# Kernel optimization log

Hardware: AMD Instinct MI355X
Metric: run time of the kernel (lower is better)

## Reference

```python
import jax, jax.numpy as jnp
import numpy as np

B, S, H, N = 1024, 200, 128, 100000  # batch, seq_len, hidden_size, num_item


def setup_inputs() -> dict:
    key = jax.random.key(0)
    ks = jax.random.split(key, 6)
    return {
        "all_memory": jax.random.normal(ks[0], (B, S, H), dtype=jnp.float32),
        "last_memory": jax.random.normal(ks[1], (B, H), dtype=jnp.float32),
        "item_seq": jax.random.randint(ks[2], (B, S), 0, N),
        "mask": jnp.zeros((B, S), dtype=jnp.bool_),
        "Ur_w": jax.random.normal(ks[3], (H, H), dtype=jnp.float32) / np.sqrt(H),
        "Wr_w": jax.random.normal(ks[4], (H, H), dtype=jnp.float32) / np.sqrt(H),
        "Vr_w": jax.random.normal(ks[5], (1, H), dtype=jnp.float32) / np.sqrt(H),
        "Vr_b": jnp.zeros((1,), dtype=jnp.float32),
    }


def reference(all_memory, last_memory, item_seq, mask, Ur_w, Wr_w, Vr_w, Vr_b):
    # torch Linear: y = x @ W.T (+ b). dropout_prob=0 -> identity.
    am = jnp.einsum("bsh,kh->bsk", all_memory, Ur_w)          # [B,S,H]
    lm = jnp.einsum("bh,kh->bk", last_memory, Wr_w)           # [B,H]
    e = jnp.tanh(am + lm[:, None, :])                          # [B,S,H]
    scores = jnp.einsum("bsh,oh->bso", e, Vr_w)[..., 0] + Vr_b  # [B,S]
    scores = jnp.where(mask, jnp.float32(-1e9), scores)
    att = jax.nn.softmax(scores, axis=-1)                      # [B,S]
    # scatter_add along item-id bins per batch row
    rows = jnp.arange(att.shape[0])[:, None]                   # [B,1]
    out = jnp.zeros((att.shape[0], N), dtype=att.dtype)
    out = out.at[rows, item_seq].add(att)                      # [B,N]
    return out
```

## Files before the change

### kernel.cpp

```cpp
#include <hip/hip_runtime.h>
#include <math.h>
#include <stdint.h>

#define BB 1024
#define SS 200
#define HH 128
#define NI 100000

typedef __attribute__((ext_vector_type(8))) short short8;
typedef __attribute__((ext_vector_type(4))) float f32x4;

__device__ __forceinline__ float fast_tanh(float x) {
    float ax = fabsf(x);
    float t = __expf(-2.0f * ax);
    float r = (1.0f - t) / (1.0f + t);
    return copysignf(r, x);
}

__device__ __forceinline__ void split8(const float* __restrict__ p,
                                       short8& hi, short8& lo) {
    const float4* p4 = reinterpret_cast<const float4*>(p);
    float4 x0 = p4[0], x1 = p4[1];
    float v[8] = {x0.x, x0.y, x0.z, x0.w, x1.x, x1.y, x1.z, x1.w};
    #pragma unroll
    for (int j = 0; j < 8; ++j) {
        unsigned u = __float_as_uint(v[j]);
        unsigned short h = (unsigned short)(u >> 16);
        hi[j] = (short)h;
        float r = v[j] - __uint_as_float(((unsigned)h) << 16);
        lo[j] = (short)(__float_as_uint(r) >> 16);
    }
}

__global__ __launch_bounds__(256, 2)
void rrd_mfma_kernel(const float* __restrict__ allm,
                     const float* __restrict__ lastm,
                     const int* __restrict__ item_seq,
                     const unsigned char* __restrict__ mask,
                     const float* __restrict__ Ur,
                     const float* __restrict__ Wr,
                     const float* __restrict__ Vr,
                     const float* __restrict__ Vrb,
                     float* __restrict__ out) {
    const int b = blockIdx.x;
    const int tid = threadIdx.x;
    const int lane = tid & 63;
    const int w = tid >> 6;
    const int col = lane & 15;
    const int quad = lane >> 4;

    __shared__ float s_last[HH];
    __shared__ float s_lm[HH];
    __shared__ float s_vr[HH];
    __shared__ float s_score[256];
    __shared__ float s_red[8];

    if (tid < HH) s_last[tid] = lastm[b * HH + tid];
    else          s_vr[tid - HH] = Vr[tid - HH];
    __syncthreads();

    if (tid < HH) {
        const float4* wrow = reinterpret_cast<const float4*>(Wr + tid * HH);
        const float4* lrow = reinterpret_cast<const float4*>(s_last);
        float4 acc = make_float4(0.f, 0.f, 0.f, 0.f);
        #pragma unroll
        for (int i = 0; i < HH / 4; ++i) {
            float4 wv = wrow[i];
            float4 lv = lrow[i];
            acc.x = fmaf(lv.x, wv.x, acc.x);
            acc.y = fmaf(lv.y, wv.y, acc.y);
            acc.z = fmaf(lv.z, wv.z, acc.z);
            acc.w = fmaf(lv.w, wv.w, acc.w);
        }
        s_lm[tid] = (acc.x + acc.y) + (acc.z + acc.w);
    }
    __syncthreads();

    const int row0 = w * 64;
    #pragma unroll 1
    for (int p = 0; p < 2; ++p) {
        f32x4 C[2][8] = {};
        #pragma unroll 1
        for (int c = 0; c < 4; ++c) {
            short8 Bh[8], Bl[8];
            #pragma unroll
            for (int n = 0; n < 8; ++n) {
                const float* bp = Ur + (size_t)(n * 16 + col) * HH + c * 32 + quad * 8;
                split8(bp, Bh[n], Bl[n]);
            }
            #pragma unroll
            for (int t = 0; t < 2; ++t) {
                int row = row0 + (p * 2 + t) * 16 + col;
                if (row > SS - 1) row = SS - 1;
                const float* ap = allm + ((size_t)b * SS + row) * HH + c * 32 + quad * 8;
                short8 Ah, Al;
                split8(ap, Ah, Al);
                #pragma unroll
                for (int n = 0; n < 8; ++n) {
                    C[t][n] = __builtin_amdgcn_mfma_f32_16x16x32_bf16(Ah, Bh[n], C[t][n], 0, 0, 0);
                    C[t][n] = __builtin_amdgcn_mfma_f32_16x16x32_bf16(Ah, Bl[n], C[t][n], 0, 0, 0);
                    C[t][n] = __builtin_amdgcn_mfma_f32_16x16x32_bf16(Al, Bh[n], C[t][n], 0, 0, 0);
                }
            }
        }
        #pragma unroll
        for (int t = 0; t < 2; ++t) {
            float a0 = 0.f, a1 = 0.f, a2 = 0.f, a3 = 0.f;
            #pragma unroll
            for (int n = 0; n < 8; ++n) {
                float lmc = s_lm[n * 16 + col];
                float vrc = s_vr[n * 16 + col];
                a0 = fmaf(vrc, fast_tanh(C[t][n][0] + lmc), a0);
                a1 = fmaf(vrc, fast_tanh(C[t][n][1] + lmc), a1);
                a2 = fmaf(vrc, fast_tanh(C[t][n][2] + lmc), a2);
                a3 = fmaf(vrc, fast_tanh(C[t][n][3] + lmc), a3);
            }
            #pragma unroll
            for (int off = 1; off < 16; off <<= 1) {
                a0 += __shfl_xor(a0, off, 64);
                a1 += __shfl_xor(a1, off, 64);
                a2 += __shfl_xor(a2, off, 64);
                a3 += __shfl_xor(a3, off, 64);
            }
            if (col == 0) {
                int rb = row0 + (p * 2 + t) * 16 + quad * 4;
                s_score[rb + 0] = a0;
                s_score[rb + 1] = a1;
                s_score[rb + 2] = a2;
                s_score[rb + 3] = a3;
            }
        }
    }

    {
        float4* orow = reinterpret_cast<float4*>(out + (size_t)b * NI);
        const float4 z4 = make_float4(0.f, 0.f, 0.f, 0.f);
        for (int i = tid; i < NI / 4; i += 256) orow[i] = z4;
    }

    __syncthreads();

    const int s = tid;
    float score = s_score[s] + Vrb[0];
    if (s < SS && mask[b * SS + s]) score = -1e9f;

    float v = (s < SS) ? score : -3.0e38f;
    #pragma unroll
    for (int off = 32; off > 0; off >>= 1)
        v = fmaxf(v, __shfl_down(v, off, 64));
    if (lane == 0) s_red[w] = v;
    __syncthreads();
    float m = fmaxf(fmaxf(s_red[0], s_red[1]), fmaxf(s_red[2], s_red[3]));

    float e = (s < SS) ? __expf(score - m) : 0.f;
    float sv = e;
    #pragma unroll
    for (int off = 32; off > 0; off >>= 1)
        sv += __shfl_down(sv, off, 64);
    if (lane == 0) s_red[4 + w] = sv;
    __syncthreads();
    float tot = (s_red[4] + s_red[5]) + (s_red[6] + s_red[7]);

    if (s < SS) {
        float att = e / tot;
        int idx = item_seq[b * SS + s];
        atomicAdd(out + (size_t)b * NI + idx, att);
    }
}

extern "C" void kernel_launch(void* const* d_in, const int* in_sizes, int n_in,
                              void* d_out, int out_size, void* d_ws, size_t ws_size,
                              hipStream_t stream) {
    const float* allm   = (const float*)d_in[0];
    const float* lastm  = (const float*)d_in[1];
    const int*   iseq   = (const int*)d_in[2];
    const unsigned char* mask = (const unsigned char*)d_in[3];
    const float* Ur     = (const float*)d_in[4];
    const float* Wr     = (const float*)d_in[5];
    const float* Vr     = (const float*)d_in[6];
    const float* Vrb    = (const float*)d_in[7];
    float* out          = (float*)d_out;

    rrd_mfma_kernel<<<dim3(BB), dim3(256), 0, stream>>>(
        allm, lastm, iseq, mask, Ur, Wr, Vr, Vrb, out);
}
```

Before: 569.0 us.

## Precompute Wr projection and Ur bf16 hi/lo split in a prep kernel

Adds a prep kernel that computes last_memory@Wr^T for all batches and pre-splits Ur into bf16 hi/lo fragments laid out in MFMA operand order in workspace. The main kernel then loads these ready-made fragments instead of redoing the Wr matvec and the Ur split in each of 1024 blocks. This removes redundant per-block ALU work and Ur reads, at the cost of an extra kernel launch and workspace traffic. It falls back to the old kernel when the workspace is too small.

```diff
diff --git a/kernel.cpp b/kernel.cpp
--- a/kernel.cpp
+++ b/kernel.cpp
@@ -29,6 +29,169 @@
         hi[j] = (short)h;
         float r = v[j] - __uint_as_float(((unsigned)h) << 16);
         lo[j] = (short)(__float_as_uint(r) >> 16);
+    }
+}
+
+__global__ __launch_bounds__(256)
+void rrd_prep_kernel(const float* __restrict__ lastm,
+                     const float* __restrict__ Wr,
+                     const float* __restrict__ Ur,
+                     float* __restrict__ lm_ws,
+                     short* __restrict__ ur_hi,
+                     short* __restrict__ ur_lo) {
+    const int blk = blockIdx.x;
+    const int tid = threadIdx.x;
+    if (blk < 512) {
+        const int gid = blk * 256 + tid;
+        const int b = gid >> 7;
+        const int k = gid & 127;
+        const float4* wrow = reinterpret_cast<const float4*>(Wr + (size_t)k * HH);
+        const float4* lrow = reinterpret_cast<const float4*>(lastm + (size_t)b * HH);
+        float4 acc = make_float4(0.f, 0.f, 0.f, 0.f);
+        #pragma unroll
+        for (int i = 0; i < HH / 4; ++i) {
+            float4 wv = wrow[i];
+            float4 lv = lrow[i];
+            acc.x = fmaf(lv.x, wv.x, acc.x);
+            acc.y = fmaf(lv.y, wv.y, acc.y);
+            acc.z = fmaf(lv.z, wv.z, acc.z);
+            acc.w = fmaf(lv.w, wv.w, acc.w);
+        }
+        lm_ws[gid] = (acc.x + acc.y) + (acc.z + acc.w);
+    } else {
+        const int r = (blk - 512) * 256 + tid;
+        const int c    = r >> 9;
+        const int n    = (r >> 6) & 7;
+        const int quad = (r >> 4) & 3;
+        const int col  = r & 15;
+        const int row = n * 16 + col;
+        const int k0  = c * 32 + quad * 8;
+        short8 hi, lo;
+        split8(Ur + (size_t)row * HH + k0, hi, lo);
+        reinterpret_cast<short8*>(ur_hi)[r] = hi;
+        reinterpret_cast<short8*>(ur_lo)[r] = lo;
+    }
+}
+
+__global__ __launch_bounds__(256, 2)
+void rrd_mfma_kernel_p(const float* __restrict__ allm,
+                       const int* __restrict__ item_seq,
+                       const unsigned char* __restrict__ mask,
+                       const short* __restrict__ ur_hi,
+                       const short* __restrict__ ur_lo,
+                       const float* __restrict__ lm_ws,
+                       const float* __restrict__ Vr,
+                       const float* __restrict__ Vrb,
+                       float* __restrict__ out) {
+    const int b = blockIdx.x;
+    const int tid = threadIdx.x;
+    const int lane = tid & 63;
+    const int w = tid >> 6;
+    const int col = lane & 15;
+    const int quad = lane >> 4;
+
+    __shared__ float s_lm[HH];
+    __shared__ float s_vr[HH];
+    __shared__ float s_score[256];
+    __shared__ float s_red[8];
+
+    if (tid < HH) s_lm[tid] = lm_ws[(size_t)b * HH + tid];
+    else          s_vr[tid - HH] = Vr[tid - HH];
+    __syncthreads();
+
+    const short8* uh = reinterpret_cast<const short8*>(ur_hi);
+    const short8* ul = reinterpret_cast<const short8*>(ur_lo);
+
+    const int row0 = w * 64;
+    #pragma unroll 1
+    for (int p = 0; p < 2; ++p) {
+        f32x4 C[2][8] = {};
+        #pragma unroll 1
+        for (int c = 0; c < 4; ++c) {
+            short8 Bh[8], Bl[8];
+            const int rbase = c * 512 + quad * 16 + col;
+            #pragma unroll
+            for (int n = 0; n < 8; ++n) {
+                Bh[n] = uh[rbase + n * 64];
+                Bl[n] = ul[rbase + n * 64];
+            }
+            #pragma unroll
+            for (int t = 0; t < 2; ++t) {
+                int row = row0 + (p * 2 + t) * 16 + col;
+                if (row > SS - 1) row = SS - 1;
+                const float* ap = allm + ((size_t)b * SS + row) * HH + c * 32 + quad * 8;
+                short8 Ah, Al;
+                split8(ap, Ah, Al);
+                #pragma unroll
+                for (int n = 0; n < 8; ++n) {
+                    C[t][n] = __builtin_amdgcn_mfma_f32_16x16x32_bf16(Ah, Bh[n], C[t][n], 0, 0, 0);
+                    C[t][n] = __builtin_amdgcn_mfma_f32_16x16x32_bf16(Ah, Bl[n], C[t][n], 0, 0, 0);
+                    C[t][n] = __builtin_amdgcn_mfma_f32_16x16x32_bf16(Al, Bh[n], C[t][n], 0, 0, 0);
+                }
+            }
+        }
+        #pragma unroll
+        for (int t = 0; t < 2; ++t) {
+            float a0 = 0.f, a1 = 0.f, a2 = 0.f, a3 = 0.f;
+            #pragma unroll
+            for (int n = 0; n < 8; ++n) {
+                float lmc = s_lm[n * 16 + col];
+                float vrc = s_vr[n * 16 + col];
+                a0 = fmaf(vrc, fast_tanh(C[t][n][0] + lmc), a0);
+                a1 = fmaf(vrc, fast_tanh(C[t][n][1] + lmc), a1);
+                a2 = fmaf(vrc, fast_tanh(C[t][n][2] + lmc), a2);
+                a3 = fmaf(vrc, fast_tanh(C[t][n][3] + lmc), a3);
+            }
+            #pragma unroll
+            for (int off = 1; off < 16; off <<= 1) {
+                a0 += __shfl_xor(a0, off, 64);
+                a1 += __shfl_xor(a1, off, 64);
+                a2 += __shfl_xor(a2, off, 64);
+                a3 += __shfl_xor(a3, off, 64);
+            }
+            if (col == 0) {
+                int rb = row0 + (p * 2 + t) * 16 + quad * 4;
+                s_score[rb + 0] = a0;
+                s_score[rb + 1] = a1;
+                s_score[rb + 2] = a2;
+                s_score[rb + 3] = a3;
+            }
+        }
+    }
+
+    {
+        float4* orow = reinterpret_cast<float4*>(out + (size_t)b * NI);
+        const float4 z4 = make_float4(0.f, 0.f, 0.f, 0.f);
+        for (int i = tid; i < NI / 4; i += 256) orow[i] = z4;
+    }
+
+    __syncthreads();
+
+    const int s = tid;
+    float score = s_score[s] + Vrb[0];
+    if (s < SS && mask[b * SS + s]) score = -1e9f;
+
+    float v = (s < SS) ? score : -3.0e38f;
+    #pragma unroll
+    for (int off = 32; off > 0; off >>= 1)
+        v = fmaxf(v, __shfl_down(v, off, 64));
+    if (lane == 0) s_red[w] = v;
+    __syncthreads();
+    float m = fmaxf(fmaxf(s_red[0], s_red[1]), fmaxf(s_red[2], s_red[3]));
+
+    float e = (s < SS) ? __expf(score - m) : 0.f;
+    float sv = e;
+    #pragma unroll
+    for (int off = 32; off > 0; off >>= 1)
+        sv += __shfl_down(sv, off, 64);
+    if (lane == 0) s_red[4 + w] = sv;
+    __syncthreads();
+    float tot = (s_red[4] + s_red[5]) + (s_red[6] + s_red[7]);
+
+    if (s < SS) {
+        float att = e / tot;
+        int idx = item_seq[b * SS + s];
+        atomicAdd(out + (size_t)b * NI + idx, att);
     }
 }
 
@@ -181,6 +344,20 @@
     const float* Vrb    = (const float*)d_in[7];
     float* out          = (float*)d_out;
 
-    rrd_mfma_kernel<<<dim3(BB), dim3(256), 0, stream>>>(
-        allm, lastm, iseq, mask, Ur, Wr, Vr, Vrb, out);
-}
+    const size_t lm_bytes = (size_t)BB * HH * sizeof(float);
+    const size_t ur_bytes = (size_t)HH * HH * sizeof(short);
+    const size_t need = lm_bytes + 2 * ur_bytes;
+
+    if (d_ws != nullptr && ws_size >= need) {
+        float* lm_ws = (float*)d_ws;
+        short* ur_hi = (short*)((char*)d_ws + lm_bytes);
+        short* ur_lo = (short*)((char*)d_ws + lm_bytes + ur_bytes);
+        rrd_prep_kernel<<<dim3(520), dim3(256), 0, stream>>>(
+            lastm, Wr, Ur, lm_ws, ur_hi, ur_lo);
+        rrd_mfma_kernel_p<<<dim3(BB), dim3(256), 0, stream>>>(
+            allm, iseq, mask, ur_hi, ur_lo, lm_ws, Vr, Vrb, out);
+    } else {
+        rrd_mfma_kernel<<<dim3(BB), dim3(256), 0, stream>>>(
+            allm, lastm, iseq, mask, Ur, Wr, Vr, Vrb, out);
+    }
+}
```

Result: faster. 525.7 us (median of 2 runs) (-7.6%).
